# Kernel optimization log

Measured on AMD Instinct MI355X. Metric: run time of the kernel, lower is better.

## Reference

```python
import jax, jax.numpy as jnp
import numpy as np

N = 65536        # total nodes (32 graphs x 2048 nodes)
E = 1048576      # total edges (avg degree 16)
D = 64           # in_dim
H = 64           # hidden_dim
O = 32           # out_dim
B = 32           # number of graphs in the batch
NPG = 2048       # nodes per graph
EPS = 1e-5
SLOPE = 0.01     # LeakyReLU negative slope


def setup_inputs() -> dict:
    key = jax.random.key(0)
    ks = jax.random.split(key, 7)
    x = jax.random.normal(ks[0], (N, D), jnp.float32)
    edge_weights = jax.random.uniform(ks[1], (E,), jnp.float32)
    src = jax.random.randint(ks[2], (E,), 0, N, dtype=jnp.int32)
    dst = jax.random.randint(ks[3], (E,), 0, N, dtype=jnp.int32)
    graph_ids = (jnp.arange(N, dtype=jnp.int32) // NPG).astype(jnp.int32)
    # DGL GraphConv weight is (in_feats, out_feats); Linear weight is (out, in)
    W1 = jax.random.normal(ks[4], (D, H), jnp.float32) * np.float32(1.0 / np.sqrt(D))
    W2 = jax.random.normal(ks[5], (H, H), jnp.float32) * np.float32(1.0 / np.sqrt(H))
    Wc = jax.random.normal(ks[6], (O, H), jnp.float32) * np.float32(1.0 / np.sqrt(H))
    gn1_w = jnp.ones((H,), jnp.float32); gn1_b = jnp.zeros((H,), jnp.float32); gn1_a = jnp.ones((H,), jnp.float32)
    gn2_w = jnp.ones((H,), jnp.float32); gn2_b = jnp.zeros((H,), jnp.float32); gn2_a = jnp.ones((H,), jnp.float32)
    return dict(x=x, edge_weights=edge_weights, W1=W1, W2=W2, Wc=Wc,
                gn1_w=gn1_w, gn1_b=gn1_b, gn1_a=gn1_a,
                gn2_w=gn2_w, gn2_b=gn2_b, gn2_a=gn2_a,
                src=src, dst=dst, graph_ids=graph_ids)


def _graph_conv(h, W, src, dst, ew, inv_sqrt_out, inv_sqrt_in):
    # DGL GraphConv norm='both' with edge_weight:
    # out = D_in^{-1/2} * scatter_sum( ew * (D_out^{-1/2} h W)[src] -> dst )
    h = (h * inv_sqrt_out[:, None]) @ W                       # [N,H]
    m = h[src] * ew[:, None]                                  # [E,H] gather + edge weight
    agg = jax.ops.segment_sum(m, dst, num_segments=N)         # [N,H] scatter
    return agg * inv_sqrt_in[:, None]


def _graph_norm(x, w, b, a):
    # GraphNorm: (x - a*mean) / sqrt(var(x - a*mean) + eps) * w + b, stats over node dim
    mean = jnp.mean(x, axis=0, keepdims=True)
    sub = x - a * mean
    std = jnp.sqrt(jnp.mean(sub * sub, axis=0, keepdims=True) + EPS)
    return w * (sub / std) + b


def _leaky(x):
    return jnp.where(x >= 0, x, SLOPE * x)


def reference(x, edge_weights, W1, W2, Wc,
              gn1_w, gn1_b, gn1_a, gn2_w, gn2_b, gn2_a,
              src, dst, graph_ids):
    ones_e = jnp.ones((E,), x.dtype)
    deg_out = jnp.maximum(jax.ops.segment_sum(ones_e, src, num_segments=N), 1.0)
    deg_in = jnp.maximum(jax.ops.segment_sum(ones_e, dst, num_segments=N), 1.0)
    inv_so = jax.lax.rsqrt(deg_out)
    inv_si = jax.lax.rsqrt(deg_in)

    h = _graph_conv(x, W1, src, dst, edge_weights, inv_so, inv_si)
    h = _graph_norm(_leaky(h), gn1_w, gn1_b, gn1_a)
    h = _graph_conv(h, W2, src, dst, edge_weights, inv_so, inv_si)
    h = _graph_norm(_leaky(h), gn2_w, gn2_b, gn2_a)

    # dgl.mean_nodes: per-graph mean pooling
    counts = jax.ops.segment_sum(jnp.ones((N,), x.dtype), graph_ids, num_segments=B)
    pooled = jax.ops.segment_sum(h, graph_ids, num_segments=B) / counts[:, None]  # [B,H]
    return pooled @ Wc.T  # [B,O]
```

## Files before the change

kernel.cpp:

```cpp
#include <hip/hip_runtime.h>

#define N_NODES 65536
#define N_EDGES 1048576
#define B_GRAPHS 32
#define NPG     2048
#define EPS_GN  1e-5f
#define SLOPE   0.01f
#define NBUCKET 256
#define STRIDE_B 4608

typedef unsigned short ushort_t;
typedef unsigned int uint_t;

static __device__ __forceinline__ ushort_t f2bf(float f) {
    uint_t u = __float_as_uint(f);
    return (ushort_t)((u + 0x7FFFu + ((u >> 16) & 1u)) >> 16);
}

static __device__ __forceinline__ void acc_bf8(float4& a0, float4& a1, uint4 u, float w) {
    a0.x += __uint_as_float(u.x << 16) * w;
    a0.y += __uint_as_float(u.x & 0xffff0000u) * w;
    a0.z += __uint_as_float(u.y << 16) * w;
    a0.w += __uint_as_float(u.y & 0xffff0000u) * w;
    a1.x += __uint_as_float(u.z << 16) * w;
    a1.y += __uint_as_float(u.z & 0xffff0000u) * w;
    a1.z += __uint_as_float(u.w << 16) * w;
    a1.w += __uint_as_float(u.w & 0xffff0000u) * w;
}

__global__ __launch_bounds__(256) void hist_kernel(const int4* __restrict__ src4,
                                                   unsigned int* __restrict__ partial,
                                                   int* __restrict__ cursor) {
    __shared__ unsigned int bins[16384];
    int tid = threadIdx.x, c = blockIdx.x;
#pragma unroll
    for (int k = 0; k < 64; ++k) bins[k * 256 + tid] = 0u;
    if (c == 0) cursor[tid] = tid * STRIDE_B;
    __syncthreads();
#pragma unroll
    for (int k = 0; k < 16; ++k) {
        int4 v = src4[c * 4096 + k * 256 + tid];
        atomicAdd(&bins[v.x >> 2], 1u << ((v.x & 3) * 8));
        atomicAdd(&bins[v.y >> 2], 1u << ((v.y & 3) * 8));
        atomicAdd(&bins[v.z >> 2], 1u << ((v.z & 3) * 8));
        atomicAdd(&bins[v.w >> 2], 1u << ((v.w & 3) * 8));
    }
    __syncthreads();
    unsigned int* dstp = partial + c * 16384;
#pragma unroll
    for (int k = 0; k < 64; ++k) dstp[k * 256 + tid] = bins[k * 256 + tid];
}

__global__ __launch_bounds__(256) void reduce_src(const unsigned int* __restrict__ partial,
                                                  float4* __restrict__ inv_so4) {
    int w = blockIdx.x * 256 + threadIdx.x;
    unsigned int s0 = 0, s1 = 0, s2 = 0, s3 = 0;
#pragma unroll
    for (int c = 0; c < 64; ++c) {
        unsigned int v = partial[c * 16384 + w];
        s0 += v & 255u; s1 += (v >> 8) & 255u; s2 += (v >> 16) & 255u; s3 += v >> 24;
    }
    float4 r;
    r.x = rsqrtf((float)max((int)s0, 1));
    r.y = rsqrtf((float)max((int)s1, 1));
    r.z = rsqrtf((float)max((int)s2, 1));
    r.w = rsqrtf((float)max((int)s3, 1));
    inv_so4[w] = r;
}

__global__ __launch_bounds__(256) void bucket_scatter(const int4* __restrict__ src4,
                                                      const int4* __restrict__ dst4,
                                                      const float4* __restrict__ ew4,
                                                      int* __restrict__ cursor,
                                                      int2* __restrict__ bedges) {
    __shared__ int lhist[NBUCKET];
    __shared__ int lstart[NBUCKET];
    __shared__ int gbase[NBUCKET];
    __shared__ int sc[NBUCKET];
    __shared__ int2 staged[2048];
    int tid = threadIdx.x;
    int vbase = blockIdx.x * 512;
    lhist[tid] = 0;
    __syncthreads();
    int w0[8]; int wbr[8]; float wwt[8];
#pragma unroll
    for (int k = 0; k < 2; ++k) {
        int4 s = src4[vbase + k * 256 + tid];
        int4 d = dst4[vbase + k * 256 + tid];
        float4 w = ew4[vbase + k * 256 + tid];
        int ss[4] = {s.x, s.y, s.z, s.w};
        int dd[4] = {d.x, d.y, d.z, d.w};
        float wf[4] = {w.x, w.y, w.z, w.w};
#pragma unroll
        for (int j = 0; j < 4; ++j) {
            int b = dd[j] >> 8;
            w0[k * 4 + j] = ss[j] | ((dd[j] & 255) << 16);
            wwt[k * 4 + j] = wf[j];
            int r = atomicAdd(&lhist[b], 1);
            wbr[k * 4 + j] = (b << 16) | r;
        }
    }
    __syncthreads();
    int cnt = lhist[tid];
    sc[tid] = cnt;
    __syncthreads();
    for (int off = 1; off < 256; off <<= 1) {
        int t = (tid >= off) ? sc[tid - off] : 0;
        __syncthreads();
        sc[tid] += t;
        __syncthreads();
    }
    lstart[tid] = sc[tid] - cnt;
    gbase[tid] = cnt ? atomicAdd(&cursor[tid], cnt) : 0;
    __syncthreads();
#pragma unroll
    for (int k = 0; k < 8; ++k)
        staged[lstart[wbr[k] >> 16] + (wbr[k] & 0xFFFF)] =
            make_int2(w0[k], __float_as_int(wwt[k]));
    __syncthreads();
    int gb = gbase[tid], ls = lstart[tid];
    for (int i = 0; i < cnt; ++i)
        bedges[gb + i] = staged[ls + i];
}

__global__ __launch_bounds__(256) void gemm_f32(const float* __restrict__ in,
                                                const float* __restrict__ W,
                                                const float* __restrict__ inv_so,
                                                ushort_t* __restrict__ out_bf) {
    __shared__ float wT[64][68];
    __shared__ float xlds[16][64];
    int tid = threadIdx.x;
#pragma unroll
    for (int j = 0; j < 16; ++j) {
        int i = j * 256 + tid;
        wT[i & 63][i >> 6] = W[i];
    }
    int r0 = blockIdx.x * 16;
#pragma unroll
    for (int j = 0; j < 4; ++j) {
        int i = j * 256 + tid;
        int r = i >> 6, k = i & 63;
        int gr = r0 + r;
        xlds[r][k] = in[(size_t)gr * 64 + k] * inv_so[gr];
    }
    __syncthreads();
    int c = tid & 63;
    int rg = tid >> 6;
    float acc[4] = {0.f, 0.f, 0.f, 0.f};
#pragma unroll
    for (int k0 = 0; k0 < 64; k0 += 4) {
        float4 wv = *(const float4*)&wT[c][k0];
#pragma unroll
        for (int j = 0; j < 4; ++j) {
            float4 xv = *(const float4*)&xlds[rg * 4 + j][k0];
            acc[j] += xv.x * wv.x + xv.y * wv.y + xv.z * wv.z + xv.w * wv.w;
        }
    }
#pragma unroll
    for (int j = 0; j < 4; ++j)
        out_bf[(size_t)(r0 + rg * 4 + j) * 64 + c] = f2bf(acc[j]);
}

__global__ __launch_bounds__(256) void gemm_bf16(const ushort_t* __restrict__ in,
                                                 const float* __restrict__ W,
                                                 const float* __restrict__ inv_so,
                                                 const float* __restrict__ alpha,
                                                 const float* __restrict__ beta,
                                                 ushort_t* __restrict__ out_bf) {
    __shared__ float wT[64][68];
    __shared__ float xlds[16][64];
    int tid = threadIdx.x;
#pragma unroll
    for (int j = 0; j < 16; ++j) {
        int i = j * 256 + tid;
        wT[i & 63][i >> 6] = W[i];
    }
    int r0 = blockIdx.x * 16;
    const uint_t* inU = (const uint_t*)in;
#pragma unroll
    for (int j = 0; j < 2; ++j) {
        int idx = j * 256 + tid;
        int r = idx >> 5, kp = idx & 31;
        int gr = r0 + r;
        uint_t u = inU[(size_t)gr * 32 + kp];
        int k0 = kp * 2;
        float lo = __uint_as_float(u << 16);
        float hi = __uint_as_float(u & 0xffff0000u);
        float iso = inv_so[gr];
        xlds[r][k0]     = (alpha[k0] * lo + beta[k0]) * iso;
        xlds[r][k0 + 1] = (alpha[k0 + 1] * hi + beta[k0 + 1]) * iso;
    }
    __syncthreads();
    int c = tid & 63;
    int rg = tid >> 6;
    float acc[4] = {0.f, 0.f, 0.f, 0.f};
#pragma unroll
    for (int k0 = 0; k0 < 64; k0 += 4) {
        float4 wv = *(const float4*)&wT[c][k0];
#pragma unroll
        for (int j = 0; j < 4; ++j) {
            float4 xv = *(const float4*)&xlds[rg * 4 + j][k0];
            acc[j] += xv.x * wv.x + xv.y * wv.y + xv.z * wv.z + xv.w * wv.w;
        }
    }
#pragma unroll
    for (int j = 0; j < 4; ++j)
        out_bf[(size_t)(r0 + rg * 4 + j) * 64 + c] = f2bf(acc[j]);
}

__global__ __launch_bounds__(1024) void agg_fused(const ushort_t* __restrict__ Tb,
                                                  const int2* __restrict__ bedges,
                                                  const int* __restrict__ cursor,
                                                  ushort_t* __restrict__ Yb,
                                                  float4* __restrict__ statsP4) {
    __shared__ int2 staged[STRIDE_B];
    __shared__ int2 sorted[STRIDE_B];
    __shared__ int hist[256];
    __shared__ int sc[256];
    __shared__ int nstart[256];
    __shared__ int ndeg[256];
    int tid = threadIdx.x, b = blockIdx.x;
    int e0 = b * STRIDE_B;
    int nE = cursor[b] - e0;
    if (tid < 256) hist[tid] = 0;
    __syncthreads();
    for (int i = tid; i < nE; i += 1024) {
        int2 e = bedges[e0 + i];
        staged[i] = e;
        atomicAdd(&hist[(e.x >> 16) & 255], 1);
    }
    __syncthreads();
    if (tid < 256) sc[tid] = hist[tid];
    __syncthreads();
    for (int off = 1; off < 256; off <<= 1) {
        int t = (tid >= off && tid < 256) ? sc[tid - off] : 0;
        __syncthreads();
        if (tid < 256) sc[tid] += t;
        __syncthreads();
    }
    if (tid < 256) {
        int cnt = hist[tid];
        int start = sc[tid] - cnt;
        nstart[tid] = start;
        ndeg[tid] = cnt;
        hist[tid] = start;
    }
    __syncthreads();
    for (int i = tid; i < nE; i += 1024) {
        int2 e = staged[i];
        int pos = atomicAdd(&hist[(e.x >> 16) & 255], 1);
        sorted[pos] = make_int2(e.x & 0xFFFF, e.y);
    }
    __syncthreads();
    const long* sl = (const long*)sorted;
    int l8 = tid & 7;
    int wv = tid >> 6;
    int ln = tid & 63;
#pragma unroll
    for (int pass = 0; pass < 2; ++pass) {
        int nl = pass * 128 + (tid >> 3);
        int node = b * 256 + nl;
        int off = nstart[nl];
        int cnt = ndeg[nl];
        float4 a0 = make_float4(0.f, 0.f, 0.f, 0.f);
        float4 a1 = make_float4(0.f, 0.f, 0.f, 0.f);
        int i = 0;
        for (; i + 8 <= cnt; i += 8) {
            long e[8];
#pragma unroll
            for (int k = 0; k < 8; ++k) e[k] = sl[off + i + k];
            uint4 t[8];
#pragma unroll
            for (int k = 0; k < 8; ++k)
                t[k] = ((const uint4*)(Tb + (((size_t)(e[k] & 0xFFFF)) << 6)))[l8];
#pragma unroll
            for (int k = 0; k < 8; ++k)
                acc_bf8(a0, a1, t[k], __int_as_float((int)(e[k] >> 32)));
        }
        for (; i < cnt; ++i) {
            long e = sl[off + i];
            uint4 u = ((const uint4*)(Tb + (((size_t)(e & 0xFFFF)) << 6)))[l8];
            acc_bf8(a0, a1, u, __int_as_float((int)(e >> 32)));
        }
        float s = rsqrtf((float)max(cnt, 1));
        float4 v0, v1;
        v0.x = a0.x * s; v0.x = (v0.x >= 0.f) ? v0.x : SLOPE * v0.x;
        v0.y = a0.y * s; v0.y = (v0.y >= 0.f) ? v0.y : SLOPE * v0.y;
        v0.z = a0.z * s; v0.z = (v0.z >= 0.f) ? v0.z : SLOPE * v0.z;
        v0.w = a0.w * s; v0.w = (v0.w >= 0.f) ? v0.w : SLOPE * v0.w;
        v1.x = a1.x * s; v1.x = (v1.x >= 0.f) ? v1.x : SLOPE * v1.x;
        v1.y = a1.y * s; v1.y = (v1.y >= 0.f) ? v1.y : SLOPE * v1.y;
        v1.z = a1.z * s; v1.z = (v1.z >= 0.f) ? v1.z : SLOPE * v1.z;
        v1.w = a1.w * s; v1.w = (v1.w >= 0.f) ? v1.w : SLOPE * v1.w;
        if (Yb) {
            uint_t p0 = (uint_t)f2bf(v0.x) | ((uint_t)f2bf(v0.y) << 16);
            uint_t p1 = (uint_t)f2bf(v0.z) | ((uint_t)f2bf(v0.w) << 16);
            uint_t p2 = (uint_t)f2bf(v1.x) | ((uint_t)f2bf(v1.y) << 16);
            uint_t p3 = (uint_t)f2bf(v1.z) | ((uint_t)f2bf(v1.w) << 16);
            ((uint4*)Yb)[(size_t)node * 8 + l8] = make_uint4(p0, p1, p2, p3);
        }
        float4 s0 = v0, s1 = v1;
        float4 q0 = make_float4(v0.x * v0.x, v0.y * v0.y, v0.z * v0.z, v0.w * v0.w);
        float4 q1 = make_float4(v1.x * v1.x, v1.y * v1.y, v1.z * v1.z, v1.w * v1.w);
#pragma unroll
        for (int m = 8; m <= 32; m <<= 1) {
            s0.x += __shfl_xor(s0.x, m); s0.y += __shfl_xor(s0.y, m);
            s0.z += __shfl_xor(s0.z, m); s0.w += __shfl_xor(s0.w, m);
            s1.x += __shfl_xor(s1.x, m); s1.y += __shfl_xor(s1.y, m);
            s1.z += __shfl_xor(s1.z, m); s1.w += __shfl_xor(s1.w, m);
            q0.x += __shfl_xor(q0.x, m); q0.y += __shfl_xor(q0.y, m);
            q0.z += __shfl_xor(q0.z, m); q0.w += __shfl_xor(q0.w, m);
            q1.x += __shfl_xor(q1.x, m); q1.y += __shfl_xor(q1.y, m);
            q1.z += __shfl_xor(q1.z, m); q1.w += __shfl_xor(q1.w, m);
        }
        if (ln < 8) {
            float4* row = statsP4 + ((size_t)b * 32 + pass * 16 + wv) * 32;
            row[ln * 2 + 0] = s0;
            row[ln * 2 + 1] = s1;
            row[16 + ln * 2 + 0] = q0;
            row[16 + ln * 2 + 1] = q1;
        }
    }
}

__global__ __launch_bounds__(256) void reduce_statsA(const float* __restrict__ statsP,
                                                     float* __restrict__ slab) {
    __shared__ float red[256];
    int tid = threadIdx.x, b = blockIdx.x;
    int col = tid & 127, half = tid >> 7;
    float s = 0.f;
    for (int i = half; i < 128; i += 2)
        s += statsP[(size_t)(b * 128 + i) * 128 + col];
    red[tid] = s;
    __syncthreads();
    if (tid < 128) slab[b * 128 + tid] = red[tid] + red[tid + 128];
}

__global__ __launch_bounds__(256) void reduce_stats2(const float* __restrict__ statsP,
                                                     float* __restrict__ slab,
                                                     float* __restrict__ pooledSum) {
    __shared__ float red[256];
    int tid = threadIdx.x, b = blockIdx.x;
    if (b < 64) {
        int col = tid & 127, half = tid >> 7;
        float s = 0.f;
        for (int i = half; i < 128; i += 2)
            s += statsP[(size_t)(b * 128 + i) * 128 + col];
        red[tid] = s;
        __syncthreads();
        if (tid < 128) slab[b * 128 + tid] = red[tid] + red[tid + 128];
    } else {
        int g = b - 64;
        int col = tid & 63, part = tid >> 6;
        float s = 0.f;
        for (int r = g * 256 + part; r < (g + 1) * 256; r += 4)
            s += statsP[(size_t)r * 128 + col];
        red[tid] = s;
        __syncthreads();
        if (tid < 64)
            pooledSum[g * 64 + tid] =
                red[tid] + red[tid + 64] + red[tid + 128] + red[tid + 192];
    }
}

__global__ void finalize_kernel(const float* __restrict__ slab,
                                const float* __restrict__ w, const float* __restrict__ b,
                                const float* __restrict__ a,
                                float* __restrict__ alpha, float* __restrict__ beta) {
    int f = threadIdx.x;
    float Sy = 0.f, Qy = 0.f;
    for (int i = 0; i < 64; ++i) {
        Sy += slab[i * 128 + f];
        Qy += slab[i * 128 + 64 + f];
    }
    float m = Sy * (1.f / N_NODES);
    float q = Qy * (1.f / N_NODES);
    float af = a[f];
    float var = q - 2.f * af * m * m + af * af * m * m;
    float al = w[f] / sqrtf(var + EPS_GN);
    alpha[f] = al;
    beta[f] = b[f] - al * af * m;
}

__global__ __launch_bounds__(256) void out_kernel(const float* __restrict__ slab2,
                                                  const float* __restrict__ gn_w,
                                                  const float* __restrict__ gn_b,
                                                  const float* __restrict__ gn_a,
                                                  const float* __restrict__ pooledSum,
                                                  const float* __restrict__ Wc,
                                                  float* __restrict__ out) {
    __shared__ float al[64], be[64];
    __shared__ float p[B_GRAPHS * 64];
    int tid = threadIdx.x;
    if (tid < 64) {
        float Sy = 0.f, Qy = 0.f;
        for (int i = 0; i < 64; ++i) {
            Sy += slab2[i * 128 + tid];
            Qy += slab2[i * 128 + 64 + tid];
        }
        float m = Sy * (1.f / N_NODES);
        float q = Qy * (1.f / N_NODES);
        float af = gn_a[tid];
        float var = q - 2.f * af * m * m + af * af * m * m;
        float a_ = gn_w[tid] / sqrtf(var + EPS_GN);
        al[tid] = a_;
        be[tid] = gn_b[tid] - a_ * af * m;
    }
    __syncthreads();
    for (int i = tid; i < B_GRAPHS * 64; i += 256) {
        int f = i & 63;
        p[i] = al[f] * (pooledSum[i] * (1.f / NPG)) + be[f];
    }
    __syncthreads();
    for (int idx = tid; idx < B_GRAPHS * 32; idx += 256) {
        int g = idx >> 5, o = idx & 31;
        float acc = 0.f;
        for (int f = 0; f < 64; ++f)
            acc += p[g * 64 + f] * Wc[o * 64 + f];
        out[idx] = acc;
    }
}

extern "C" void kernel_launch(void* const* d_in, const int* in_sizes, int n_in,
                              void* d_out, int out_size, void* d_ws, size_t ws_size,
                              hipStream_t stream) {
    const float* x     = (const float*)d_in[0];
    const float* ew    = (const float*)d_in[1];
    const float* W1    = (const float*)d_in[2];
    const float* W2    = (const float*)d_in[3];
    const float* Wc    = (const float*)d_in[4];
    const float* gn1_w = (const float*)d_in[5];
    const float* gn1_b = (const float*)d_in[6];
    const float* gn1_a = (const float*)d_in[7];
    const float* gn2_w = (const float*)d_in[8];
    const float* gn2_b = (const float*)d_in[9];
    const float* gn2_a = (const float*)d_in[10];
    const int* src     = (const int*)d_in[11];
    const int* dst     = (const int*)d_in[12];

    char* ws = (char*)d_ws;
    int*   cursor    = (int*)(ws + 0);
    float* ab1       = (float*)(ws + 4096);
    float* pooledSum = (float*)(ws + 8192);
    float* slab1     = (float*)(ws + 16384);
    float* slab2     = (float*)(ws + 49152);
    float* inv_so    = (float*)(ws + 655360);
    unsigned int* partial = (unsigned int*)(ws + (2u << 20));
    int2*  bedges    = (int2*)(ws + (10u << 20));
    ushort_t* Tbf    = (ushort_t*)(ws + (20u << 20));
    ushort_t* Ybf    = (ushort_t*)(ws + (28u << 20));
    float* statsP    = (float*)(ws + (36u << 20));

    hist_kernel<<<64, 256, 0, stream>>>((const int4*)src, partial, cursor);
    reduce_src<<<64, 256, 0, stream>>>(partial, (float4*)inv_so);
    bucket_scatter<<<512, 256, 0, stream>>>((const int4*)src, (const int4*)dst,
                                            (const float4*)ew, cursor, bedges);

    gemm_f32<<<N_NODES / 16, 256, 0, stream>>>(x, W1, inv_so, Tbf);
    agg_fused<<<NBUCKET, 1024, 0, stream>>>(Tbf, bedges, cursor, Ybf, (float4*)statsP);
    reduce_statsA<<<64, 256, 0, stream>>>(statsP, slab1);
    finalize_kernel<<<1, 64, 0, stream>>>(slab1, gn1_w, gn1_b, gn1_a, ab1 + 0, ab1 + 64);

    gemm_bf16<<<N_NODES / 16, 256, 0, stream>>>(Ybf, W2, inv_so, ab1 + 0, ab1 + 64, Tbf);
    agg_fused<<<NBUCKET, 1024, 0, stream>>>(Tbf, bedges, cursor, nullptr, (float4*)statsP);
    reduce_stats2<<<96, 256, 0, stream>>>(statsP, slab2, pooledSum);

    out_kernel<<<1, 256, 0, stream>>>(slab2, gn2_w, gn2_b, gn2_a, pooledSum, Wc,
                                      (float*)d_out);
}
```

Baseline: 165.9 us.

## Use 512 buckets, precompute per-node offsets once, enlarge GEMM row tiles

```diff
diff --git a/kernel.cpp b/kernel.cpp
--- a/kernel.cpp
+++ b/kernel.cpp
@@ -6,8 +6,8 @@
 #define NPG     2048
 #define EPS_GN  1e-5f
 #define SLOPE   0.01f
-#define NBUCKET 256
-#define STRIDE_B 4608
+#define NBUCKET 512
+#define STRIDE_B 2432
 
 typedef unsigned short ushort_t;
 typedef unsigned int uint_t;
@@ -35,7 +35,10 @@
     int tid = threadIdx.x, c = blockIdx.x;
 #pragma unroll
     for (int k = 0; k < 64; ++k) bins[k * 256 + tid] = 0u;
-    if (c == 0) cursor[tid] = tid * STRIDE_B;
+    if (c == 0) {
+        cursor[tid] = tid * STRIDE_B;
+        cursor[256 + tid] = (256 + tid) * STRIDE_B;
+    }
     __syncthreads();
 #pragma unroll
     for (int k = 0; k < 16; ++k) {
@@ -76,15 +79,16 @@
     __shared__ int lhist[NBUCKET];
     __shared__ int lstart[NBUCKET];
     __shared__ int gbase[NBUCKET];
-    __shared__ int sc[NBUCKET];
-    __shared__ int2 staged[2048];
+    __shared__ int scA[256], scB[256];
+    __shared__ int2 staged[4096];
     int tid = threadIdx.x;
-    int vbase = blockIdx.x * 512;
+    int vbase = blockIdx.x * 1024;
     lhist[tid] = 0;
-    __syncthreads();
-    int w0[8]; int wbr[8]; float wwt[8];
-#pragma unroll
-    for (int k = 0; k < 2; ++k) {
+    lhist[tid + 256] = 0;
+    __syncthreads();
+    int w0[16]; int wbr[16]; float wwt[16];
+#pragma unroll
+    for (int k = 0; k < 4; ++k) {
         int4 s = src4[vbase + k * 256 + tid];
         int4 d = dst4[vbase + k * 256 + tid];
         float4 w = ew4[vbase + k * 256 + tid];
@@ -93,34 +97,71 @@
         float wf[4] = {w.x, w.y, w.z, w.w};
 #pragma unroll
         for (int j = 0; j < 4; ++j) {
-            int b = dd[j] >> 8;
-            w0[k * 4 + j] = ss[j] | ((dd[j] & 255) << 16);
+            int b = dd[j] >> 7;
+            w0[k * 4 + j] = ss[j] | ((dd[j] & 127) << 16);
             wwt[k * 4 + j] = wf[j];
             int r = atomicAdd(&lhist[b], 1);
             wbr[k * 4 + j] = (b << 16) | r;
         }
     }
     __syncthreads();
-    int cnt = lhist[tid];
-    sc[tid] = cnt;
+    int cntA = lhist[tid], cntB = lhist[tid + 256];
+    scA[tid] = cntA;
+    scB[tid] = cntB;
     __syncthreads();
     for (int off = 1; off < 256; off <<= 1) {
-        int t = (tid >= off) ? sc[tid - off] : 0;
-        __syncthreads();
-        sc[tid] += t;
-        __syncthreads();
-    }
-    lstart[tid] = sc[tid] - cnt;
-    gbase[tid] = cnt ? atomicAdd(&cursor[tid], cnt) : 0;
-    __syncthreads();
-#pragma unroll
-    for (int k = 0; k < 8; ++k)
+        int tA = (tid >= off) ? scA[tid - off] : 0;
+        int tB = (tid >= off) ? scB[tid - off] : 0;
+        __syncthreads();
+        scA[tid] += tA;
+        scB[tid] += tB;
+        __syncthreads();
+    }
+    int lowtot = scA[255];
+    lstart[tid] = scA[tid] - cntA;
+    lstart[tid + 256] = lowtot + scB[tid] - cntB;
+    gbase[tid] = cntA ? atomicAdd(&cursor[tid], cntA) : 0;
+    gbase[tid + 256] = cntB ? atomicAdd(&cursor[tid + 256], cntB) : 0;
+    __syncthreads();
+#pragma unroll
+    for (int k = 0; k < 16; ++k)
         staged[lstart[wbr[k] >> 16] + (wbr[k] & 0xFFFF)] =
             make_int2(w0[k], __float_as_int(wwt[k]));
     __syncthreads();
-    int gb = gbase[tid], ls = lstart[tid];
-    for (int i = 0; i < cnt; ++i)
-        bedges[gb + i] = staged[ls + i];
+    {
+        int gb = gbase[tid], ls = lstart[tid];
+        for (int i = 0; i < cntA; ++i) bedges[gb + i] = staged[ls + i];
+        gb = gbase[tid + 256]; ls = lstart[tid + 256];
+        for (int i = 0; i < cntB; ++i) bedges[gb + i] = staged[ls + i];
+    }
+}
+
+__global__ __launch_bounds__(256) void refine_lite(const int* __restrict__ bedges_x,
+                                                   const int* __restrict__ cursor,
+                                                   int* __restrict__ nstart,
+                                                   int* __restrict__ ndeg) {
+    __shared__ int hist[128], sc[128];
+    int tid = threadIdx.x, b = blockIdx.x;
+    int e0 = b * STRIDE_B;
+    int nE = cursor[b] - e0;
+    if (tid < 128) hist[tid] = 0;
+    __syncthreads();
+    for (int i = tid; i < nE; i += 256)
+        atomicAdd(&hist[(bedges_x[2 * (e0 + i)] >> 16) & 127], 1);
+    __syncthreads();
+    if (tid < 128) sc[tid] = hist[tid];
+    __syncthreads();
+    for (int off = 1; off < 128; off <<= 1) {
+        int t = (tid >= off && tid < 128) ? sc[tid - off] : 0;
+        __syncthreads();
+        if (tid < 128) sc[tid] += t;
+        __syncthreads();
+    }
+    if (tid < 128) {
+        int cnt = hist[tid];
+        nstart[b * 128 + tid] = sc[tid] - cnt;
+        ndeg[b * 128 + tid] = cnt;
+    }
 }
 
 __global__ __launch_bounds__(256) void gemm_f32(const float* __restrict__ in,
@@ -128,16 +169,16 @@
                                                 const float* __restrict__ inv_so,
                                                 ushort_t* __restrict__ out_bf) {
     __shared__ float wT[64][68];
-    __shared__ float xlds[16][64];
+    __shared__ float xlds[64][64];
     int tid = threadIdx.x;
 #pragma unroll
     for (int j = 0; j < 16; ++j) {
         int i = j * 256 + tid;
         wT[i & 63][i >> 6] = W[i];
     }
-    int r0 = blockIdx.x * 16;
-#pragma unroll
-    for (int j = 0; j < 4; ++j) {
+    int r0 = blockIdx.x * 64;
+#pragma unroll
+    for (int j = 0; j < 16; ++j) {
         int i = j * 256 + tid;
         int r = i >> 6, k = i & 63;
         int gr = r0 + r;
@@ -146,19 +187,21 @@
     __syncthreads();
     int c = tid & 63;
     int rg = tid >> 6;
-    float acc[4] = {0.f, 0.f, 0.f, 0.f};
+    float acc[16];
+#pragma unroll
+    for (int j = 0; j < 16; ++j) acc[j] = 0.f;
 #pragma unroll
     for (int k0 = 0; k0 < 64; k0 += 4) {
         float4 wv = *(const float4*)&wT[c][k0];
 #pragma unroll
-        for (int j = 0; j < 4; ++j) {
-            float4 xv = *(const float4*)&xlds[rg * 4 + j][k0];
+        for (int j = 0; j < 16; ++j) {
+            float4 xv = *(const float4*)&xlds[rg * 16 + j][k0];
             acc[j] += xv.x * wv.x + xv.y * wv.y + xv.z * wv.z + xv.w * wv.w;
         }
     }
 #pragma unroll
-    for (int j = 0; j < 4; ++j)
-        out_bf[(size_t)(r0 + rg * 4 + j) * 64 + c] = f2bf(acc[j]);
+    for (int j = 0; j < 16; ++j)
+        out_bf[(size_t)(r0 + rg * 16 + j) * 64 + c] = f2bf(acc[j]);
 }
 
 __global__ __launch_bounds__(256) void gemm_bf16(const ushort_t* __restrict__ in,
@@ -168,17 +211,17 @@
                                                  const float* __restrict__ beta,
                                                  ushort_t* __restrict__ out_bf) {
     __shared__ float wT[64][68];
-    __shared__ float xlds[16][64];
+    __shared__ float xlds[64][64];
     int tid = threadIdx.x;
 #pragma unroll
     for (int j = 0; j < 16; ++j) {
         int i = j * 256 + tid;
         wT[i & 63][i >> 6] = W[i];
     }
-    int r0 = blockIdx.x * 16;
+    int r0 = blockIdx.x * 64;
     const uint_t* inU = (const uint_t*)in;
 #pragma unroll
-    for (int j = 0; j < 2; ++j) {
+    for (int j = 0; j < 8; ++j) {
         int idx = j * 256 + tid;
         int r = idx >> 5, kp = idx & 31;
         int gr = r0 + r;
@@ -193,133 +236,113 @@
     __syncthreads();
     int c = tid & 63;
     int rg = tid >> 6;
-    float acc[4] = {0.f, 0.f, 0.f, 0.f};
+    float acc[16];
+#pragma unroll
+    for (int j = 0; j < 16; ++j) acc[j] = 0.f;
 #pragma unroll
     for (int k0 = 0; k0 < 64; k0 += 4) {
         float4 wv = *(const float4*)&wT[c][k0];
 #pragma unroll
-        for (int j = 0; j < 4; ++j) {
-            float4 xv = *(const float4*)&xlds[rg * 4 + j][k0];
+        for (int j = 0; j < 16; ++j) {
+            float4 xv = *(const float4*)&xlds[rg * 16 + j][k0];
             acc[j] += xv.x * wv.x + xv.y * wv.y + xv.z * wv.z + xv.w * wv.w;
         }
     }
 #pragma unroll
-    for (int j = 0; j < 4; ++j)
-        out_bf[(size_t)(r0 + rg * 4 + j) * 64 + c] = f2bf(acc[j]);
-}
-
-__global__ __launch_bounds__(1024) void agg_fused(const ushort_t* __restrict__ Tb,
-                                                  const int2* __restrict__ bedges,
-                                                  const int* __restrict__ cursor,
-                                                  ushort_t* __restrict__ Yb,
-                                                  float4* __restrict__ statsP4) {
-    __shared__ int2 staged[STRIDE_B];
+    for (int j = 0; j < 16; ++j)
+        out_bf[(size_t)(r0 + rg * 16 + j) * 64 + c] = f2bf(acc[j]);
+}
+
+__global__ __launch_bounds__(1024, 8) void agg_bucket(const ushort_t* __restrict__ Tb,
+                                                      const int2* __restrict__ bedges,
+                                                      const int* __restrict__ cursor,
+                                                      const int* __restrict__ nstart,
+                                                      const int* __restrict__ ndeg,
+                                                      ushort_t* __restrict__ Yb,
+                                                      float4* __restrict__ statsP4) {
     __shared__ int2 sorted[STRIDE_B];
-    __shared__ int hist[256];
-    __shared__ int sc[256];
-    __shared__ int nstart[256];
-    __shared__ int ndeg[256];
+    __shared__ int nst[128], ndg[128], scur[128];
     int tid = threadIdx.x, b = blockIdx.x;
     int e0 = b * STRIDE_B;
     int nE = cursor[b] - e0;
-    if (tid < 256) hist[tid] = 0;
+    if (tid < 128) {
+        int st = nstart[b * 128 + tid];
+        nst[tid] = st;
+        scur[tid] = st;
+        ndg[tid] = ndeg[b * 128 + tid];
+    }
     __syncthreads();
     for (int i = tid; i < nE; i += 1024) {
         int2 e = bedges[e0 + i];
-        staged[i] = e;
-        atomicAdd(&hist[(e.x >> 16) & 255], 1);
-    }
-    __syncthreads();
-    if (tid < 256) sc[tid] = hist[tid];
-    __syncthreads();
-    for (int off = 1; off < 256; off <<= 1) {
-        int t = (tid >= off && tid < 256) ? sc[tid - off] : 0;
-        __syncthreads();
-        if (tid < 256) sc[tid] += t;
-        __syncthreads();
-    }
-    if (tid < 256) {
-        int cnt = hist[tid];
-        int start = sc[tid] - cnt;
-        nstart[tid] = start;
-        ndeg[tid] = cnt;
-        hist[tid] = start;
-    }
-    __syncthreads();
-    for (int i = tid; i < nE; i += 1024) {
-        int2 e = staged[i];
-        int pos = atomicAdd(&hist[(e.x >> 16) & 255], 1);
+        int dl = (e.x >> 16) & 127;
+        int pos = atomicAdd(&scur[dl], 1);
         sorted[pos] = make_int2(e.x & 0xFFFF, e.y);
     }
     __syncthreads();
     const long* sl = (const long*)sorted;
     int l8 = tid & 7;
-    int wv = tid >> 6;
-    int ln = tid & 63;
-#pragma unroll
-    for (int pass = 0; pass < 2; ++pass) {
-        int nl = pass * 128 + (tid >> 3);
-        int node = b * 256 + nl;
-        int off = nstart[nl];
-        int cnt = ndeg[nl];
-        float4 a0 = make_float4(0.f, 0.f, 0.f, 0.f);
-        float4 a1 = make_float4(0.f, 0.f, 0.f, 0.f);
-        int i = 0;
-        for (; i + 8 <= cnt; i += 8) {
-            long e[8];
-#pragma unroll
-            for (int k = 0; k < 8; ++k) e[k] = sl[off + i + k];
-            uint4 t[8];
-#pragma unroll
-            for (int k = 0; k < 8; ++k)
-                t[k] = ((const uint4*)(Tb + (((size_t)(e[k] & 0xFFFF)) << 6)))[l8];
-#pragma unroll
-            for (int k = 0; k < 8; ++k)
-                acc_bf8(a0, a1, t[k], __int_as_float((int)(e[k] >> 32)));
-        }
-        for (; i < cnt; ++i) {
-            long e = sl[off + i];
-            uint4 u = ((const uint4*)(Tb + (((size_t)(e & 0xFFFF)) << 6)))[l8];
-            acc_bf8(a0, a1, u, __int_as_float((int)(e >> 32)));
-        }
-        float s = rsqrtf((float)max(cnt, 1));
-        float4 v0, v1;
-        v0.x = a0.x * s; v0.x = (v0.x >= 0.f) ? v0.x : SLOPE * v0.x;
-        v0.y = a0.y * s; v0.y = (v0.y >= 0.f) ? v0.y : SLOPE * v0.y;
-        v0.z = a0.z * s; v0.z = (v0.z >= 0.f) ? v0.z : SLOPE * v0.z;
-        v0.w = a0.w * s; v0.w = (v0.w >= 0.f) ? v0.w : SLOPE * v0.w;
-        v1.x = a1.x * s; v1.x = (v1.x >= 0.f) ? v1.x : SLOPE * v1.x;
-        v1.y = a1.y * s; v1.y = (v1.y >= 0.f) ? v1.y : SLOPE * v1.y;
-        v1.z = a1.z * s; v1.z = (v1.z >= 0.f) ? v1.z : SLOPE * v1.z;
-        v1.w = a1.w * s; v1.w = (v1.w >= 0.f) ? v1.w : SLOPE * v1.w;
-        if (Yb) {
-            uint_t p0 = (uint_t)f2bf(v0.x) | ((uint_t)f2bf(v0.y) << 16);
-            uint_t p1 = (uint_t)f2bf(v0.z) | ((uint_t)f2bf(v0.w) << 16);
-            uint_t p2 = (uint_t)f2bf(v1.x) | ((uint_t)f2bf(v1.y) << 16);
-            uint_t p3 = (uint_t)f2bf(v1.z) | ((uint_t)f2bf(v1.w) << 16);
-            ((uint4*)Yb)[(size_t)node * 8 + l8] = make_uint4(p0, p1, p2, p3);
-        }
-        float4 s0 = v0, s1 = v1;
-        float4 q0 = make_float4(v0.x * v0.x, v0.y * v0.y, v0.z * v0.z, v0.w * v0.w);
-        float4 q1 = make_float4(v1.x * v1.x, v1.y * v1.y, v1.z * v1.z, v1.w * v1.w);
-#pragma unroll
-        for (int m = 8; m <= 32; m <<= 1) {
-            s0.x += __shfl_xor(s0.x, m); s0.y += __shfl_xor(s0.y, m);
-            s0.z += __shfl_xor(s0.z, m); s0.w += __shfl_xor(s0.w, m);
-            s1.x += __shfl_xor(s1.x, m); s1.y += __shfl_xor(s1.y, m);
-            s1.z += __shfl_xor(s1.z, m); s1.w += __shfl_xor(s1.w, m);
-            q0.x += __shfl_xor(q0.x, m); q0.y += __shfl_xor(q0.y, m);
-            q0.z += __shfl_xor(q0.z, m); q0.w += __shfl_xor(q0.w, m);
-            q1.x += __shfl_xor(q1.x, m); q1.y += __shfl_xor(q1.y, m);
-            q1.z += __shfl_xor(q1.z, m); q1.w += __shfl_xor(q1.w, m);
-        }
-        if (ln < 8) {
-            float4* row = statsP4 + ((size_t)b * 32 + pass * 16 + wv) * 32;
-            row[ln * 2 + 0] = s0;
-            row[ln * 2 + 1] = s1;
-            row[16 + ln * 2 + 0] = q0;
-            row[16 + ln * 2 + 1] = q1;
-        }
+    int nl = tid >> 3;
+    int node = b * 128 + nl;
+    int off = nst[nl];
+    int cnt = ndg[nl];
+    float4 a0 = make_float4(0.f, 0.f, 0.f, 0.f);
+    float4 a1 = make_float4(0.f, 0.f, 0.f, 0.f);
+    int i = 0;
+    for (; i + 8 <= cnt; i += 8) {
+        long e[8];
+#pragma unroll
+        for (int k = 0; k < 8; ++k) e[k] = sl[off + i + k];
+        uint4 t[8];
+#pragma unroll
+        for (int k = 0; k < 8; ++k)
+            t[k] = ((const uint4*)(Tb + (((size_t)(e[k] & 0xFFFF)) << 6)))[l8];
+#pragma unroll
+        for (int k = 0; k < 8; ++k)
+            acc_bf8(a0, a1, t[k], __int_as_float((int)(e[k] >> 32)));
+    }
+    for (; i < cnt; ++i) {
+        long e = sl[off + i];
+        uint4 u = ((const uint4*)(Tb + (((size_t)(e & 0xFFFF)) << 6)))[l8];
+        acc_bf8(a0, a1, u, __int_as_float((int)(e >> 32)));
+    }
+    float s = rsqrtf((float)max(cnt, 1));
+    float4 v0, v1;
+    v0.x = a0.x * s; v0.x = (v0.x >= 0.f) ? v0.x : SLOPE * v0.x;
+    v0.y = a0.y * s; v0.y = (v0.y >= 0.f) ? v0.y : SLOPE * v0.y;
+    v0.z = a0.z * s; v0.z = (v0.z >= 0.f) ? v0.z : SLOPE * v0.z;
+    v0.w = a0.w * s; v0.w = (v0.w >= 0.f) ? v0.w : SLOPE * v0.w;
+    v1.x = a1.x * s; v1.x = (v1.x >= 0.f) ? v1.x : SLOPE * v1.x;
+    v1.y = a1.y * s; v1.y = (v1.y >= 0.f) ? v1.y : SLOPE * v1.y;
+    v1.z = a1.z * s; v1.z = (v1.z >= 0.f) ? v1.z : SLOPE * v1.z;
+    v1.w = a1.w * s; v1.w = (v1.w >= 0.f) ? v1.w : SLOPE * v1.w;
+    if (Yb) {
+        uint_t p0 = (uint_t)f2bf(v0.x) | ((uint_t)f2bf(v0.y) << 16);
+        uint_t p1 = (uint_t)f2bf(v0.z) | ((uint_t)f2bf(v0.w) << 16);
+        uint_t p2 = (uint_t)f2bf(v1.x) | ((uint_t)f2bf(v1.y) << 16);
+        uint_t p3 = (uint_t)f2bf(v1.z) | ((uint_t)f2bf(v1.w) << 16);
+        ((uint4*)Yb)[(size_t)node * 8 + l8] = make_uint4(p0, p1, p2, p3);
+    }
+    float4 s0 = v0, s1 = v1;
+    float4 q0 = make_float4(v0.x * v0.x, v0.y * v0.y, v0.z * v0.z, v0.w * v0.w);
+    float4 q1 = make_float4(v1.x * v1.x, v1.y * v1.y, v1.z * v1.z, v1.w * v1.w);
+#pragma unroll
+    for (int m = 8; m <= 32; m <<= 1) {
+        s0.x += __shfl_xor(s0.x, m); s0.y += __shfl_xor(s0.y, m);
+        s0.z += __shfl_xor(s0.z, m); s0.w += __shfl_xor(s0.w, m);
+        s1.x += __shfl_xor(s1.x, m); s1.y += __shfl_xor(s1.y, m);
+        s1.z += __shfl_xor(s1.z, m); s1.w += __shfl_xor(s1.w, m);
+        q0.x += __shfl_xor(q0.x, m); q0.y += __shfl_xor(q0.y, m);
+        q0.z += __shfl_xor(q0.z, m); q0.w += __shfl_xor(q0.w, m);
+        q1.x += __shfl_xor(q1.x, m); q1.y += __shfl_xor(q1.y, m);
+        q1.z += __shfl_xor(q1.z, m); q1.w += __shfl_xor(q1.w, m);
+    }
+    int wv = tid >> 6, ln = tid & 63;
+    if (ln < 8) {
+        float4* row = statsP4 + ((size_t)b * 16 + wv) * 32;
+        row[ln * 2 + 0] = s0;
+        row[ln * 2 + 1] = s1;
+        row[16 + ln * 2 + 0] = q0;
+        row[16 + ln * 2 + 1] = q1;
     }
 }
 
@@ -444,6 +467,8 @@
     float* pooledSum = (float*)(ws + 8192);
     float* slab1     = (float*)(ws + 16384);
     float* slab2     = (float*)(ws + 49152);
+    int*   nstart    = (int*)(ws + 131072);
+    int*   ndeg      = (int*)(ws + 393216);
     float* inv_so    = (float*)(ws + 655360);
     unsigned int* partial = (unsigned int*)(ws + (2u << 20));
     int2*  bedges    = (int2*)(ws + (10u << 20));
@@ -453,16 +478,19 @@
 
     hist_kernel<<<64, 256, 0, stream>>>((const int4*)src, partial, cursor);
     reduce_src<<<64, 256, 0, stream>>>(partial, (float4*)inv_so);
-    bucket_scatter<<<512, 256, 0, stream>>>((const int4*)src, (const int4*)dst,
+    bucket_scatter<<<256, 256, 0, stream>>>((const int4*)src, (const int4*)dst,
                                             (const float4*)ew, cursor, bedges);
-
-    gemm_f32<<<N_NODES / 16, 256, 0, stream>>>(x, W1, inv_so, Tbf);
-    agg_fused<<<NBUCKET, 1024, 0, stream>>>(Tbf, bedges, cursor, Ybf, (float4*)statsP);
+    refine_lite<<<NBUCKET, 256, 0, stream>>>((const int*)bedges, cursor, nstart, ndeg);
+
+    gemm_f32<<<N_NODES / 64, 256, 0, stream>>>(x, W1, inv_so, Tbf);
+    agg_bucket<<<NBUCKET, 1024, 0, stream>>>(Tbf, bedges, cursor, nstart, ndeg,
+                                             Ybf, (float4*)statsP);
     reduce_statsA<<<64, 256, 0, stream>>>(statsP, slab1);
     finalize_kernel<<<1, 64, 0, stream>>>(slab1, gn1_w, gn1_b, gn1_a, ab1 + 0, ab1 + 64);
 
-    gemm_bf16<<<N_NODES / 16, 256, 0, stream>>>(Ybf, W2, inv_so, ab1 + 0, ab1 + 64, Tbf);
-    agg_fused<<<NBUCKET, 1024, 0, stream>>>(Tbf, bedges, cursor, nullptr, (float4*)statsP);
+    gemm_bf16<<<N_NODES / 64, 256, 0, stream>>>(Ybf, W2, inv_so, ab1 + 0, ab1 + 64, Tbf);
+    agg_bucket<<<NBUCKET, 1024, 0, stream>>>(Tbf, bedges, cursor, nstart, ndeg,
+                                             nullptr, (float4*)statsP);
     reduce_stats2<<<96, 256, 0, stream>>>(statsP, slab2, pooledSum);
 
     out_kernel<<<1, 256, 0, stream>>>(slab2, gn2_w, gn2_b, gn2_a, pooledSum, Wc,
```

After: 155.3 us. 6.4% less time.
